# Optimization experiments

Measured on AMD Instinct MI355X. Metric: run time of the kernel, lower is better.

## Reference

```python
import jax, jax.numpy as jnp
import numpy as np

B, S, D = 4, 2048, 1024
LN_EPS = 1e-3  # keras LayerNormalization default


def setup_inputs() -> dict:
    key = jax.random.key(0)
    ks = jax.random.split(key, 4)
    std = 1.0 / np.sqrt(D)
    return {
        "inputs": jax.random.normal(ks[0], (B, S, D), dtype=jnp.float32),
        "Wq": jax.random.normal(ks[1], (D, D), dtype=jnp.float32) * std,
        "bq": jnp.zeros((D,), jnp.float32),
        "Wk": jax.random.normal(ks[2], (D, D), dtype=jnp.float32) * std,
        "bk": jnp.zeros((D,), jnp.float32),
        "Wv": jax.random.normal(ks[3], (D, D), dtype=jnp.float32) * std,
        "bv": jnp.zeros((D,), jnp.float32),
        "ln_gamma": jnp.ones((D,), jnp.float32),
        "ln_beta": jnp.zeros((D,), jnp.float32),
    }


def reference(inputs, Wq, bq, Wk, bk, Wv, bv, ln_gamma, ln_beta):
    d = inputs.shape[-1]
    scale = jnp.sqrt(jnp.asarray(d, inputs.dtype))
    q = inputs @ Wq + bq          # [B,S,D]
    k = inputs @ Wk + bk
    v = inputs @ Wv + bv
    scores = jnp.einsum("bqd,bkd->bqk", q, k) / scale  # [B,S,S]
    attn = jax.nn.softmax(scores, axis=-1)
    context = jnp.einsum("bqk,bkd->bqd", attn, v)      # [B,S,D]
    resid = context + inputs
    mu = jnp.mean(resid, axis=-1, keepdims=True)
    var = jnp.mean(jnp.square(resid - mu), axis=-1, keepdims=True)
    normed = (resid - mu) * jax.lax.rsqrt(var + LN_EPS)
    return normed * ln_gamma + ln_beta
```

## Files before the change

### kernel.cpp

```cpp
#include <hip/hip_runtime.h>
#include <hip/hip_bf16.h>
#include <cstdint>
#include <cstddef>


typedef unsigned short u16;
using bf16x8 = __attribute__((ext_vector_type(8))) short;
using f32x4  = __attribute__((ext_vector_type(4))) float;

typedef __attribute__((address_space(3))) unsigned int lds_uint;
typedef const __attribute__((address_space(1))) unsigned int glob_uint;

__device__ __forceinline__ float bf2f(u16 h) {
    union { unsigned int u; float f; } c;
    c.u = ((unsigned int)h) << 16;
    return c.f;
}
__device__ __forceinline__ u16 f2bf(float f) {
    union { float f; unsigned int u; } c;
    c.f = f;
    return (u16)((c.u + 0x7fffu + ((c.u >> 16) & 1u)) >> 16);
}
__device__ __forceinline__ void load_lds16(const void* g, void* l) {
    __builtin_amdgcn_global_load_lds((glob_uint*)g, (lds_uint*)l, 16, 0, 0);
}

__global__ void detect_mode_kernel(const u16* __restrict__ X, int* __restrict__ flag)
{
    const int lane = threadIdx.x;
    bool bad = false, nz = false;
    for (int j = 0; j < 4; ++j) {
        float v = bf2f(X[(lane * 4 + j) * 2]);
        if (!(fabsf(v) <= 1e9f)) bad = true;
        if (v != 0.f) nz = true;
    }
    unsigned long long anybad = __ballot(bad);
    unsigned long long anynz  = __ballot(nz);
    if (lane == 0) *flag = (anybad != 0ull || anynz == 0ull) ? 1 : 0;
}

__global__ __launch_bounds__(256) void convert_small_kernel(
    const void* s0, const void* s1, const void* s2, const void* s3,
    const void* s4, u16* __restrict__ dst, const int* __restrict__ flag)
{
    const void* srcs[5] = {s0, s1, s2, s3, s4};
    const void* src = srcs[blockIdx.x];
    u16* d = dst + (size_t)blockIdx.x * 1024;
    const int i = threadIdx.x * 4;
    if (*flag) {
        const float* f = (const float*)src;
        ushort4 o;
        o.x = f2bf(f[i]); o.y = f2bf(f[i + 1]);
        o.z = f2bf(f[i + 2]); o.w = f2bf(f[i + 3]);
        *(ushort4*)(d + i) = o;
    } else {
        *(ushort4*)(d + i) = *(const ushort4*)((const u16*)src + i);
    }
}

__global__ __launch_bounds__(256) void convert_x_kernel(
    const void* __restrict__ X, u16* __restrict__ Xb, const int* __restrict__ flag)
{
    const size_t i = ((size_t)blockIdx.x * 256 + threadIdx.x) * 8;
    if (*flag) {
        const float* f = (const float*)X;
        float4 a = *(const float4*)(f + i);
        float4 b = *(const float4*)(f + i + 4);
        ushort4 o0, o1;
        o0.x = f2bf(a.x); o0.y = f2bf(a.y); o0.z = f2bf(a.z); o0.w = f2bf(a.w);
        o1.x = f2bf(b.x); o1.y = f2bf(b.y); o1.z = f2bf(b.z); o1.w = f2bf(b.w);
        *(ushort4*)(Xb + i) = o0;
        *(ushort4*)(Xb + i + 4) = o1;
    } else {
        *(uint4*)(Xb + i) = *(const uint4*)((const u16*)X + i);
    }
}

__global__ __launch_bounds__(256) void transpose_w_kernel(
    const void* __restrict__ Wq, const void* __restrict__ Wk,
    const void* __restrict__ Wv, u16* __restrict__ Wt,
    const int* __restrict__ flag)
{
    __shared__ u16 tile[64][72];
    const int t  = threadIdx.x;
    const int k0 = blockIdx.x * 64;
    const int n0 = blockIdx.y * 64;
    const int w  = blockIdx.z;
    const void* W = (w == 0) ? Wq : ((w == 1) ? Wk : Wv);
    const int fp32 = *flag;
#pragma unroll
    for (int it = 0; it < 2; ++it) {
        int idx = t + it * 256;
        int r = idx >> 3;
        int c = (idx & 7) * 8;
        const size_t off = (size_t)(k0 + r) * 1024 + n0 + c;
        if (fp32) {
            const float* Wf = (const float*)W + off;
            float4 a = *(const float4*)Wf;
            float4 b = *(const float4*)(Wf + 4);
            u16* tp = &tile[r][c];
            tp[0] = f2bf(a.x); tp[1] = f2bf(a.y); tp[2] = f2bf(a.z); tp[3] = f2bf(a.w);
            tp[4] = f2bf(b.x); tp[5] = f2bf(b.y); tp[6] = f2bf(b.z); tp[7] = f2bf(b.w);
        } else {
            *(uint4*)&tile[r][c] = *(const uint4*)((const u16*)W + off);
        }
    }
    __syncthreads();
#pragma unroll
    for (int it = 0; it < 2; ++it) {
        int idx = t + it * 256;
        int r = idx >> 3;
        int c = (idx & 7) * 8;
        union { u16 s[8]; uint4 v; } tmp;
#pragma unroll
        for (int j = 0; j < 8; ++j) tmp.s[j] = tile[c + j][r];
        *(uint4*)(Wt + (size_t)(w * 1024 + n0 + r) * 1024 + k0 + c) = tmp.v;
    }
}

__global__ __launch_bounds__(256) void transpose_v4_kernel(
    const u16* __restrict__ QKV, u16* __restrict__ Vt4)
{
    __shared__ u16 tile[64][72];
    const int t  = threadIdx.x;
    const int k0 = blockIdx.x * 64;
    const int n0 = blockIdx.y * 64;
    const int b  = blockIdx.z;
    const u16* Vsrc = QKV + (size_t)b * 2048 * 3072 + 2048;
    u16* Vt = Vt4 + (size_t)b * 1024 * 2048;
#pragma unroll
    for (int it = 0; it < 2; ++it) {
        int idx = t + it * 256;
        int r = idx >> 3;
        int c = (idx & 7) * 8;
        *(uint4*)&tile[r][c] = *(const uint4*)(Vsrc + (size_t)(k0 + r) * 3072 + n0 + c);
    }
    __syncthreads();
#pragma unroll
    for (int it = 0; it < 2; ++it) {
        int idx = t + it * 256;
        int r = idx >> 3;
        int c = (idx & 7) * 8;
        union { u16 s[8]; uint4 v; } tmp;
#pragma unroll
        for (int j = 0; j < 8; ++j) tmp.s[j] = tile[c + j][r];
        *(uint4*)(Vt + (size_t)(n0 + r) * 2048 + k0 + c) = tmp.v;
    }
}

template<int EPI>
__global__ __launch_bounds__(256) void gemm128(
    const u16* __restrict__ A, int lda, size_t sA,
    const u16* __restrict__ Bt, int ldb, size_t sB,
    u16* __restrict__ C, int ldc, size_t sC,
    int K, float scale, const u16* __restrict__ bias3)
{
    __shared__ u16 As[128 * 32];
    __shared__ u16 Bs[128 * 32];
    const int t    = threadIdx.x;
    const int lane = t & 63;
    const int w    = t >> 6;
    const int wr   = w >> 1, wc = w & 1;
    const int quad = lane >> 4, l16 = lane & 15;
    const int m0 = blockIdx.y * 128;
    const int n0 = blockIdx.x * 128;
    const int b  = blockIdx.z;
    A  += (size_t)b * sA;
    Bt += (size_t)b * sB;
    C  += (size_t)b * sC;

    const int srow = lane >> 2;
    const int scol = (lane & 3) * 8;
    const u16* Ag0 = A  + (size_t)(m0 + w * 32 +      srow) * lda + scol;
    const u16* Ag1 = A  + (size_t)(m0 + w * 32 + 16 + srow) * lda + scol;
    const u16* Bg0 = Bt + (size_t)(n0 + w * 32 +      srow) * ldb + scol;
    const u16* Bg1 = Bt + (size_t)(n0 + w * 32 + 16 + srow) * ldb + scol;
    u16* Al0 = As + (w * 32) * 32;
    u16* Al1 = As + (w * 32 + 16) * 32;
    u16* Bl0 = Bs + (w * 32) * 32;
    u16* Bl1 = Bs + (w * 32 + 16) * 32;

    f32x4 acc[4][4];
#pragma unroll
    for (int mi = 0; mi < 4; ++mi)
#pragma unroll
        for (int ni = 0; ni < 4; ++ni)
            acc[mi][ni] = (f32x4){0.f, 0.f, 0.f, 0.f};

    for (int k0 = 0; k0 < K; k0 += 32) {
        load_lds16(Ag0 + k0, Al0);
        load_lds16(Ag1 + k0, Al1);
        load_lds16(Bg0 + k0, Bl0);
        load_lds16(Bg1 + k0, Bl1);
        __syncthreads();
        bf16x8 af[4], bfr[4];
#pragma unroll
        for (int i = 0; i < 4; ++i) {
            af[i]  = *(const bf16x8*)&As[(wr * 64 + i * 16 + l16) * 32 + quad * 8];
            bfr[i] = *(const bf16x8*)&Bs[(wc * 64 + i * 16 + l16) * 32 + quad * 8];
        }
#pragma unroll
        for (int mi = 0; mi < 4; ++mi)
#pragma unroll
            for (int ni = 0; ni < 4; ++ni)
                acc[mi][ni] = __builtin_amdgcn_mfma_f32_16x16x32_bf16(
                    af[mi], bfr[ni], acc[mi][ni], 0, 0, 0);
        __syncthreads();
    }

    const int row0 = m0 + wr * 64 + quad * 4;
    const int col0 = n0 + wc * 64 + l16;
#pragma unroll
    for (int mi = 0; mi < 4; ++mi) {
#pragma unroll
        for (int ni = 0; ni < 4; ++ni) {
            const int col = col0 + ni * 16;
            const float bias = (EPI == 0) ? bf2f(bias3[col]) : 0.f;
#pragma unroll
            for (int r = 0; r < 4; ++r) {
                const int row = row0 + mi * 16 + r;
                C[(size_t)row * ldc + col] = f2bf(acc[mi][ni][r] * scale + bias);
            }
        }
    }
}

__global__ __launch_bounds__(256) void softmax_bf16_kernel(u16* __restrict__ S)
{
    const int t = threadIdx.x;
    u16* sp = S + (size_t)blockIdx.x * 2048;
    union { uint4 v; u16 h[8]; } raw;
    raw.v = *(const uint4*)(sp + t * 8);
    float vals[8];
#pragma unroll
    for (int i = 0; i < 8; ++i) vals[i] = bf2f(raw.h[i]);
    float m = vals[0];
#pragma unroll
    for (int i = 1; i < 8; ++i) m = fmaxf(m, vals[i]);
#pragma unroll
    for (int off = 32; off > 0; off >>= 1) m = fmaxf(m, __shfl_xor(m, off));
    __shared__ float red[8];
    const int w = t >> 6, lane = t & 63;
    if (lane == 0) red[w] = m;
    __syncthreads();
    m = fmaxf(fmaxf(red[0], red[1]), fmaxf(red[2], red[3]));
    float e[8], s = 0.f;
#pragma unroll
    for (int i = 0; i < 8; ++i) { e[i] = __expf(vals[i] - m); s += e[i]; }
#pragma unroll
    for (int off = 32; off > 0; off >>= 1) s += __shfl_xor(s, off);
    if (lane == 0) red[4 + w] = s;
    __syncthreads();
    s = red[4] + red[5] + red[6] + red[7];
    const float rinv = 1.f / s;
    union { uint4 v; u16 h[8]; } out;
#pragma unroll
    for (int i = 0; i < 8; ++i) out.h[i] = f2bf(e[i] * rinv);
    *(uint4*)(sp + t * 8) = out.v;
}

__global__ __launch_bounds__(256) void resid_ln_kernel(
    const u16* __restrict__ Ctx, const u16* __restrict__ Xb,
    const u16* __restrict__ gamma, const u16* __restrict__ beta,
    void* __restrict__ Out, const int* __restrict__ flag)
{
    const size_t row = blockIdx.x;
    const int t = threadIdx.x;
    ushort4 cv = *(const ushort4*)(Ctx + row * 3072 + t * 4);
    ushort4 xv = *(const ushort4*)(Xb + row * 1024 + t * 4);
    float v[4] = {bf2f(cv.x) + bf2f(xv.x), bf2f(cv.y) + bf2f(xv.y),
                  bf2f(cv.z) + bf2f(xv.z), bf2f(cv.w) + bf2f(xv.w)};
    float s  = v[0] + v[1] + v[2] + v[3];
    float s2 = v[0] * v[0] + v[1] * v[1] + v[2] * v[2] + v[3] * v[3];
#pragma unroll
    for (int off = 32; off > 0; off >>= 1) {
        s  += __shfl_xor(s, off);
        s2 += __shfl_xor(s2, off);
    }
    __shared__ float red[8];
    const int w = t >> 6, lane = t & 63;
    if (lane == 0) { red[w] = s; red[4 + w] = s2; }
    __syncthreads();
    s  = red[0] + red[1] + red[2] + red[3];
    s2 = red[4] + red[5] + red[6] + red[7];
    const float mu  = s * (1.f / 1024.f);
    const float var = s2 * (1.f / 1024.f) - mu * mu;
    const float inv = rsqrtf(var + 1e-3f);
    ushort4 gv = *(const ushort4*)(gamma + t * 4);
    ushort4 bv = *(const ushort4*)(beta + t * 4);
    float o[4];
    o[0] = (v[0] - mu) * inv * bf2f(gv.x) + bf2f(bv.x);
    o[1] = (v[1] - mu) * inv * bf2f(gv.y) + bf2f(bv.y);
    o[2] = (v[2] - mu) * inv * bf2f(gv.z) + bf2f(bv.z);
    o[3] = (v[3] - mu) * inv * bf2f(gv.w) + bf2f(bv.w);
    if (*flag) {
        float4 fo = {o[0], o[1], o[2], o[3]};
        *(float4*)((float*)Out + row * 1024 + t * 4) = fo;
    } else {
        ushort4 bo;
        bo.x = f2bf(o[0]); bo.y = f2bf(o[1]); bo.z = f2bf(o[2]); bo.w = f2bf(o[3]);
        *(ushort4*)((u16*)Out + row * 1024 + t * 4) = bo;
    }
}

extern "C" void kernel_launch(void* const* d_in, const int* in_sizes, int n_in,
                              void* d_out, int out_size, void* d_ws, size_t ws_size,
                              hipStream_t stream)
{
    (void)in_sizes; (void)n_in; (void)out_size; (void)ws_size;
    const void* X     = d_in[0];
    const void* Wq    = d_in[1];
    const void* bq    = d_in[2];
    const void* Wk    = d_in[3];
    const void* bk    = d_in[4];
    const void* Wv    = d_in[5];
    const void* bv    = d_in[6];
    const void* gamma = d_in[7];
    const void* beta  = d_in[8];

    char* ws = (char*)d_ws;
    int* flag  = (int*)(ws + 0);
    u16* bias5 = (u16*)(ws + 16);
    u16* Wt    = (u16*)(ws + 16384);
    u16* QKV   = (u16*)(ws + 6307840);
    u16* Xb    = (u16*)(ws + 56639488);
    u16* S4    = (u16*)(ws + 73416704);
    u16* Vt4   = (u16*)(ws + 106971136);

    detect_mode_kernel<<<1, 64, 0, stream>>>((const u16*)X, flag);
    convert_small_kernel<<<5, 256, 0, stream>>>(bq, bk, bv, gamma, beta, bias5, flag);
    convert_x_kernel<<<4096, 256, 0, stream>>>(X, Xb, flag);
    transpose_w_kernel<<<dim3(16, 16, 3), 256, 0, stream>>>(Wq, Wk, Wv, Wt, flag);

    gemm128<0><<<dim3(24, 64, 1), 256, 0, stream>>>(
        Xb, 1024, 0, Wt, 1024, 0, QKV, 3072, 0, 1024, 1.f, bias5);

    gemm128<1><<<dim3(16, 16, 4), 256, 0, stream>>>(
        QKV, 3072, (size_t)2048 * 3072,
        QKV + 1024, 3072, (size_t)2048 * 3072,
        S4, 2048, (size_t)2048 * 2048, 1024, 0.03125f, nullptr);

    softmax_bf16_kernel<<<8192, 256, 0, stream>>>(S4);
    transpose_v4_kernel<<<dim3(32, 16, 4), 256, 0, stream>>>(QKV, Vt4);

    gemm128<1><<<dim3(8, 16, 4), 256, 0, stream>>>(
        S4, 2048, (size_t)2048 * 2048,
        Vt4, 2048, (size_t)1024 * 2048,
        QKV, 3072, (size_t)2048 * 3072, 2048, 1.f, nullptr);

    resid_ln_kernel<<<8192, 256, 0, stream>>>(
        QKV, Xb, bias5 + 3 * 1024, bias5 + 4 * 1024, d_out, flag);
}
```

Baseline: 332.5 us.

## Use 32x32x16 MFMA with XOR-swizzled LDS and K=64 per barrier in GEMM

Switches the 128x128 GEMM tile's inner product from 16x16x32 MFMAs to 32x32x16 bf16 MFMAs with 2x2 accumulators per wave. This halves LDS fragment reads per flop. Global-to-LDS loads now place k-groups in an XOR-swizzled order to reduce LDS bank conflicts. Each loop iteration stages two 32-wide K slabs, halving the number of barriers. The epilogue row and column mapping changes to match the 32x32 accumulator layout, which risks layout errors and raises LDS usage.

```diff
diff --git a/kernel.cpp b/kernel.cpp
--- a/kernel.cpp
+++ b/kernel.cpp
@@ -6,7 +6,7 @@
 
 typedef unsigned short u16;
 using bf16x8 = __attribute__((ext_vector_type(8))) short;
-using f32x4  = __attribute__((ext_vector_type(4))) float;
+using f32x16 = __attribute__((ext_vector_type(16))) float;
 
 typedef __attribute__((address_space(3))) unsigned int lds_uint;
 typedef const __attribute__((address_space(1))) unsigned int glob_uint;
@@ -155,70 +155,84 @@
     u16* __restrict__ C, int ldc, size_t sC,
     int K, float scale, const u16* __restrict__ bias3)
 {
-    __shared__ u16 As[128 * 32];
-    __shared__ u16 Bs[128 * 32];
+    __shared__ u16 As[2][128 * 32];
+    __shared__ u16 Bs[2][128 * 32];
     const int t    = threadIdx.x;
     const int lane = t & 63;
     const int w    = t >> 6;
     const int wr   = w >> 1, wc = w & 1;
-    const int quad = lane >> 4, l16 = lane & 15;
     const int m0 = blockIdx.y * 128;
     const int n0 = blockIdx.x * 128;
-    const int b  = blockIdx.z;
-    A  += (size_t)b * sA;
-    Bt += (size_t)b * sB;
-    C  += (size_t)b * sC;
+    A  += (size_t)blockIdx.z * sA;
+    Bt += (size_t)blockIdx.z * sB;
+    C  += (size_t)blockIdx.z * sC;
 
     const int srow = lane >> 2;
-    const int scol = (lane & 3) * 8;
-    const u16* Ag0 = A  + (size_t)(m0 + w * 32 +      srow) * lda + scol;
-    const u16* Ag1 = A  + (size_t)(m0 + w * 32 + 16 + srow) * lda + scol;
-    const u16* Bg0 = Bt + (size_t)(n0 + w * 32 +      srow) * ldb + scol;
-    const u16* Bg1 = Bt + (size_t)(n0 + w * 32 + 16 + srow) * ldb + scol;
-    u16* Al0 = As + (w * 32) * 32;
-    u16* Al1 = As + (w * 32 + 16) * 32;
-    u16* Bl0 = Bs + (w * 32) * 32;
-    u16* Bl1 = Bs + (w * 32 + 16) * 32;
-
-    f32x4 acc[4][4];
-#pragma unroll
-    for (int mi = 0; mi < 4; ++mi)
-#pragma unroll
-        for (int ni = 0; ni < 4; ++ni)
-            acc[mi][ni] = (f32x4){0.f, 0.f, 0.f, 0.f};
-
-    for (int k0 = 0; k0 < K; k0 += 32) {
-        load_lds16(Ag0 + k0, Al0);
-        load_lds16(Ag1 + k0, Al1);
-        load_lds16(Bg0 + k0, Bl0);
-        load_lds16(Bg1 + k0, Bl1);
+    const int skg  = (lane & 3) ^ (srow & 3);
+    const u16* Ag0 = A  + (size_t)(m0 + w * 32 +      srow) * lda + skg * 8;
+    const u16* Ag1 = A  + (size_t)(m0 + w * 32 + 16 + srow) * lda + skg * 8;
+    const u16* Bg0 = Bt + (size_t)(n0 + w * 32 +      srow) * ldb + skg * 8;
+    const u16* Bg1 = Bt + (size_t)(n0 + w * 32 + 16 + srow) * ldb + skg * 8;
+    u16* Al0 = &As[0][(w * 32) * 32];
+    u16* Al1 = &As[1][(w * 32) * 32];
+    u16* Bl0 = &Bs[0][(w * 32) * 32];
+    u16* Bl1 = &Bs[1][(w * 32) * 32];
+
+    f32x16 acc[2][2];
+#pragma unroll
+    for (int mi = 0; mi < 2; ++mi)
+#pragma unroll
+        for (int ni = 0; ni < 2; ++ni)
+#pragma unroll
+            for (int r = 0; r < 16; ++r)
+                acc[mi][ni][r] = 0.f;
+
+    const int ml   = lane & 31;
+    const int kh   = lane >> 5;
+    const int lxor = lane & 3;
+
+    for (int k0 = 0; k0 < K; k0 += 64) {
+        load_lds16(Ag0 + k0,      Al0);
+        load_lds16(Ag1 + k0,      Al0 + 16 * 32);
+        load_lds16(Bg0 + k0,      Bl0);
+        load_lds16(Bg1 + k0,      Bl0 + 16 * 32);
+        load_lds16(Ag0 + k0 + 32, Al1);
+        load_lds16(Ag1 + k0 + 32, Al1 + 16 * 32);
+        load_lds16(Bg0 + k0 + 32, Bl1);
+        load_lds16(Bg1 + k0 + 32, Bl1 + 16 * 32);
         __syncthreads();
-        bf16x8 af[4], bfr[4];
-#pragma unroll
-        for (int i = 0; i < 4; ++i) {
-            af[i]  = *(const bf16x8*)&As[(wr * 64 + i * 16 + l16) * 32 + quad * 8];
-            bfr[i] = *(const bf16x8*)&Bs[(wc * 64 + i * 16 + l16) * 32 + quad * 8];
+#pragma unroll
+        for (int slab = 0; slab < 2; ++slab) {
+            const u16* as_ = As[slab];
+            const u16* bs_ = Bs[slab];
+#pragma unroll
+            for (int s = 0; s < 2; ++s) {
+                const int g    = s * 2 + kh;
+                const int slot = (g ^ lxor) * 8;
+                bf16x8 a0 = *(const bf16x8*)&as_[(wr * 64 +      ml) * 32 + slot];
+                bf16x8 a1 = *(const bf16x8*)&as_[(wr * 64 + 32 + ml) * 32 + slot];
+                bf16x8 b0 = *(const bf16x8*)&bs_[(wc * 64 +      ml) * 32 + slot];
+                bf16x8 b1 = *(const bf16x8*)&bs_[(wc * 64 + 32 + ml) * 32 + slot];
+                acc[0][0] = __builtin_amdgcn_mfma_f32_32x32x16_bf16(a0, b0, acc[0][0], 0, 0, 0);
+                acc[0][1] = __builtin_amdgcn_mfma_f32_32x32x16_bf16(a0, b1, acc[0][1], 0, 0, 0);
+                acc[1][0] = __builtin_amdgcn_mfma_f32_32x32x16_bf16(a1, b0, acc[1][0], 0, 0, 0);
+                acc[1][1] = __builtin_amdgcn_mfma_f32_32x32x16_bf16(a1, b1, acc[1][1], 0, 0, 0);
+            }
         }
-#pragma unroll
-        for (int mi = 0; mi < 4; ++mi)
-#pragma unroll
-            for (int ni = 0; ni < 4; ++ni)
-                acc[mi][ni] = __builtin_amdgcn_mfma_f32_16x16x32_bf16(
-                    af[mi], bfr[ni], acc[mi][ni], 0, 0, 0);
         __syncthreads();
     }
 
-    const int row0 = m0 + wr * 64 + quad * 4;
-    const int col0 = n0 + wc * 64 + l16;
-#pragma unroll
-    for (int mi = 0; mi < 4; ++mi) {
-#pragma unroll
-        for (int ni = 0; ni < 4; ++ni) {
-            const int col = col0 + ni * 16;
+    const int colb = n0 + wc * 64 + ml;
+    const int rowb = m0 + wr * 64 + 4 * kh;
+#pragma unroll
+    for (int mi = 0; mi < 2; ++mi) {
+#pragma unroll
+        for (int ni = 0; ni < 2; ++ni) {
+            const int col = colb + ni * 32;
             const float bias = (EPI == 0) ? bf2f(bias3[col]) : 0.f;
 #pragma unroll
-            for (int r = 0; r < 4; ++r) {
-                const int row = row0 + mi * 16 + r;
+            for (int r = 0; r < 16; ++r) {
+                const int row = rowb + mi * 32 + (r & 3) + 8 * (r >> 2);
                 C[(size_t)row * ldc + col] = f2bf(acc[mi][ni][r] * scale + bias);
             }
         }
```

New measurement: 305.1 us. -8.2%, faster.
